# Kernel optimization log

Measured on AMD Instinct MI355X. Metric: run time of the kernel, lower is better.

Reference implementation:

```python
import jax, jax.numpy as jnp
import numpy as np

EPSILON = 1e-19
MASKING_RATIO = 0.75
N_BINS = 64
SIGMA = 0.01


def setup_inputs() -> dict:
    key = jax.random.key(0)
    k1, k2 = jax.random.split(key)
    N, L, D = 4, 512, 1024
    P = 768  # 16*16*3 pixels per patch
    x = jax.random.normal(k1, (N, L, D), dtype=jnp.float32)
    img_pat = jax.random.uniform(k2, (N, L, P), dtype=jnp.float32)
    return {"x": x, "img_pat": img_pat}


def _entropy_kde(values, n_bins=N_BINS, sigma=SIGMA):
    # values: [N, L, P]; global min/max normalization as in the torch code
    bins = jnp.linspace(0.0, 1.0, n_bins, dtype=values.dtype)  # [B]
    vmin = values.min()
    vmax = values.max()
    nv = (values - vmin) / (vmax - vmin)
    # residuals: [N, L, B, P]
    resid = nv[:, :, None, :] - bins[None, None, :, None]
    kern = jnp.exp(-0.5 * (resid / sigma) ** 2)
    pdf = kern.mean(axis=3)  # [N, L, B]
    pdf = pdf / (pdf.sum(axis=2, keepdims=True) + EPSILON) + EPSILON
    return -jnp.sum(pdf * jnp.log(pdf), axis=-1)  # [N, L]


def reference(x, img_pat):
    # entropy_kde_masking branch of MaskingModule.forward
    N, L, D = x.shape
    len_keep = int(L * (1.0 - MASKING_RATIO))
    entropies = _entropy_kde(img_pat)                 # [N, L]
    ids_shuffle = jnp.argsort(entropies, axis=1)      # ascending (descending=False)
    ids_restore = jnp.argsort(ids_shuffle, axis=1)    # [N, L]
    ids_keep = ids_shuffle[:, :len_keep]              # [N, len_keep]
    x_masked = jnp.take_along_axis(x, ids_keep[:, :, None], axis=1)  # [N, len_keep, D]
    mask = jnp.ones((N, L), dtype=x.dtype).at[:, :len_keep].set(0.0)
    mask = jnp.take_along_axis(mask, ids_restore, axis=1)
    return (x_masked, mask, ids_restore)
```

## Files before the change

### kernel.cpp

```cpp
#include <hip/hip_runtime.h>

#define NB 4
#define LB 512
#define DB 1024
#define PB 768
#define NBINS 64
#define LEN_KEEP 128
#define EPSL 1e-19f
#define WIN 3

#if defined(__has_builtin)
#if __has_builtin(__builtin_amdgcn_exp2f)
#define HAVE_EXP2 1
#endif
#endif

__device__ __forceinline__ float fast_exp2(float x) {
#ifdef HAVE_EXP2
    return __builtin_amdgcn_exp2f(x);
#else
    return __expf(x * 0.69314718055994530942f);
#endif
}

__global__ void minmax_partial(const float4* __restrict__ v,
                               float* __restrict__ bmin, float* __restrict__ bmax) {
    __shared__ float smin[256], smax[256];
    int tid = threadIdx.x;
    int base = blockIdx.x * 256 + tid;
    float mn = 1e30f, mx = -1e30f;
#pragma unroll
    for (int k = 0; k < 24; ++k) {
        float4 t4 = v[base + k * 16384];
        mn = fminf(mn, fminf(fminf(t4.x, t4.y), fminf(t4.z, t4.w)));
        mx = fmaxf(mx, fmaxf(fmaxf(t4.x, t4.y), fmaxf(t4.z, t4.w)));
    }
    smin[tid] = mn; smax[tid] = mx;
    __syncthreads();
    for (int s = 128; s > 0; s >>= 1) {
        if (tid < s) {
            smin[tid] = fminf(smin[tid], smin[tid + s]);
            smax[tid] = fmaxf(smax[tid], smax[tid + s]);
        }
        __syncthreads();
    }
    if (tid == 0) { bmin[blockIdx.x] = smin[0]; bmax[blockIdx.x] = smax[0]; }
}

__global__ void entropy_kernel(const float* __restrict__ img,
                               const float* __restrict__ bmin,
                               const float* __restrict__ bmax,
                               float* __restrict__ ent) {
    __shared__ float sh[256];
    __shared__ float snv[PB];
    __shared__ int   cnt[NBINS];
    __shared__ int   bs[NBINS + 1];
    __shared__ int   pos[NBINS];

    int t = blockIdx.x;
    int tid = threadIdx.x;
    int lane = tid & 63;
    int w = tid >> 6;

    if (tid < NBINS) cnt[tid] = 0;
    if (tid < 64) {
        float mn = bmin[tid], mx = bmax[tid];
        for (int m = 1; m < 64; m <<= 1) {
            mn = fminf(mn, __shfl_xor(mn, m, 64));
            mx = fmaxf(mx, __shfl_xor(mx, m, 64));
        }
        if (tid == 0) { sh[0] = mn; sh[1] = mx; }
    }
    __syncthreads();
    float vmin = sh[0], vmax = sh[1];
    float inv = 1.0f / (vmax - vmin);

    const float* row = img + (size_t)t * PB;
    float nv0 = (row[tid]       - vmin) * inv;
    float nv1 = (row[tid + 256] - vmin) * inv;
    float nv2 = (row[tid + 512] - vmin) * inv;
    int m0 = min(63, max(0, __float2int_rn(nv0 * 63.0f)));
    int m1 = min(63, max(0, __float2int_rn(nv1 * 63.0f)));
    int m2 = min(63, max(0, __float2int_rn(nv2 * 63.0f)));
    atomicAdd(&cnt[m0], 1);
    atomicAdd(&cnt[m1], 1);
    atomicAdd(&cnt[m2], 1);
    __syncthreads();

    if (tid < 64) {
        int c = cnt[tid];
        int incl = c;
        for (int off = 1; off < 64; off <<= 1) {
            int up = __shfl_up(incl, off, 64);
            if (tid >= off) incl += up;
        }
        bs[tid + 1] = incl;
        pos[tid] = incl - c;
        if (tid == 0) bs[0] = 0;
    }
    __syncthreads();

    snv[atomicAdd(&pos[m0], 1)] = nv0;
    snv[atomicAdd(&pos[m1], 1)] = nv1;
    snv[atomicAdd(&pos[m2], 1)] = nv2;
    __syncthreads();

    float bv = (float)lane * (1.0f / 63.0f);
    int lo = bs[max(0, lane - WIN)];
    int hi = bs[min(NBINS, lane + WIN + 1)];
    const float negC = -7213.4755859375f;
    float acc = 0.0f;
    for (int j = lo + w; j < hi; j += 4) {
        float d = snv[j] - bv;
        acc += fast_exp2(d * d * negC);
    }
    sh[w * NBINS + lane] = acc;
    __syncthreads();

    if (tid < 64) {
        float pdf = (sh[lane] + sh[64 + lane] + sh[128 + lane] + sh[192 + lane])
                    * (1.0f / (float)PB);
        float s = pdf;
        for (int m = 1; m < 64; m <<= 1) s += __shfl_xor(s, m, 64);
        float p = pdf / (s + EPSL) + EPSL;
        float term = p * __logf(p);
        for (int m = 1; m < 64; m <<= 1) term += __shfl_xor(term, m, 64);
        if (tid == 0) ent[t] = -term;
    }
}

__global__ void rank_gather_kernel(const float* __restrict__ x,
                                   const float* __restrict__ ent,
                                   float* __restrict__ out_x,
                                   float* __restrict__ out_mask,
                                   float* __restrict__ out_rest) {
    __shared__ float sh[LB];
    __shared__ int keep_list[16];
    __shared__ int nkeep;
    int b = blockIdx.x, tid = threadIdx.x;
    int n = b >> 5;
    int i = (b & 31) * 16 + (tid >> 4);
    int slice = tid & 15;

    if (tid == 0) nkeep = 0;
    sh[tid]       = ent[n * LB + tid];
    sh[256 + tid] = ent[n * LB + 256 + tid];
    __syncthreads();

    unsigned long long ci =
        ((unsigned long long)__float_as_uint(sh[i]) << 32) | (unsigned int)i;
    int r = 0;
    int j0 = slice * 32;
#pragma unroll 8
    for (int j = j0; j < j0 + 32; ++j) {
        unsigned long long cj =
            ((unsigned long long)__float_as_uint(sh[j]) << 32) | (unsigned int)j;
        r += (cj < ci) ? 1 : 0;
    }
    r += __shfl_xor(r, 1, 64);
    r += __shfl_xor(r, 2, 64);
    r += __shfl_xor(r, 4, 64);
    r += __shfl_xor(r, 8, 64);
    if (slice == 0) {
        out_rest[n * LB + i] = (float)r;
        out_mask[n * LB + i] = (r < LEN_KEEP) ? 0.0f : 1.0f;
        if (r < LEN_KEEP) {
            int e = atomicAdd(&nkeep, 1);
            keep_list[e] = (r << 16) | i;
        }
    }
    __syncthreads();

    int nk = nkeep;
    for (int e = 0; e < nk; ++e) {
        int ent_ri = keep_list[e];
        int slot = ent_ri >> 16;
        int rowi = ent_ri & 0xFFFF;
        const float4* src = (const float4*)(x + ((size_t)(n * LB + rowi)) * DB);
        float4* dst = (float4*)(out_x + ((size_t)(n * LEN_KEEP + slot)) * DB);
        dst[tid] = src[tid];
    }
}

extern "C" void kernel_launch(void* const* d_in, const int* in_sizes, int n_in,
                              void* d_out, int out_size, void* d_ws, size_t ws_size,
                              hipStream_t stream) {
    const float* x   = (const float*)d_in[0];
    const float* img = (const float*)d_in[1];

    float* out      = (float*)d_out;
    float* out_x    = out;
    float* out_mask = out + (size_t)NB * LEN_KEEP * DB;
    float* out_rest = out_mask + NB * LB;

    float* ws   = (float*)d_ws;
    float* bmin = ws;
    float* bmax = ws + 64;
    float* ent  = ws + 128;

    minmax_partial<<<64, 256, 0, stream>>>((const float4*)img, bmin, bmax);
    entropy_kernel<<<NB * LB, 256, 0, stream>>>(img, bmin, bmax, ent);
    rank_gather_kernel<<<128, 256, 0, stream>>>(x, ent, out_x, out_mask, out_rest);
}
```

Baseline: 75.83 us.

## Shrink entropy kernel to one wavefront per row

After: 80.72 us. +6.4%, slower.

```diff
diff --git a/kernel.cpp b/kernel.cpp
--- a/kernel.cpp
+++ b/kernel.cpp
@@ -47,62 +47,56 @@
     if (tid == 0) { bmin[blockIdx.x] = smin[0]; bmax[blockIdx.x] = smax[0]; }
 }
 
-__global__ void entropy_kernel(const float* __restrict__ img,
-                               const float* __restrict__ bmin,
-                               const float* __restrict__ bmax,
-                               float* __restrict__ ent) {
-    __shared__ float sh[256];
+__global__ __launch_bounds__(64) void entropy_kernel(
+    const float* __restrict__ img,
+    const float* __restrict__ bmin,
+    const float* __restrict__ bmax,
+    float* __restrict__ ent) {
     __shared__ float snv[PB];
     __shared__ int   cnt[NBINS];
     __shared__ int   bs[NBINS + 1];
     __shared__ int   pos[NBINS];
 
     int t = blockIdx.x;
-    int tid = threadIdx.x;
-    int lane = tid & 63;
-    int w = tid >> 6;
+    int lane = threadIdx.x;
 
-    if (tid < NBINS) cnt[tid] = 0;
-    if (tid < 64) {
-        float mn = bmin[tid], mx = bmax[tid];
-        for (int m = 1; m < 64; m <<= 1) {
-            mn = fminf(mn, __shfl_xor(mn, m, 64));
-            mx = fmaxf(mx, __shfl_xor(mx, m, 64));
-        }
-        if (tid == 0) { sh[0] = mn; sh[1] = mx; }
+    float vmin = bmin[lane], vmax = bmax[lane];
+    for (int m = 1; m < 64; m <<= 1) {
+        vmin = fminf(vmin, __shfl_xor(vmin, m, 64));
+        vmax = fmaxf(vmax, __shfl_xor(vmax, m, 64));
+    }
+    float inv = 1.0f / (vmax - vmin);
+
+    cnt[lane] = 0;
+    __syncthreads();
+
+    const float* row = img + (size_t)t * PB;
+    float nv[12];
+    int   mb[12];
+#pragma unroll
+    for (int k = 0; k < 12; ++k) {
+        nv[k] = (row[lane + 64 * k] - vmin) * inv;
+        mb[k] = min(63, max(0, __float2int_rn(nv[k] * 63.0f)));
+        atomicAdd(&cnt[mb[k]], 1);
     }
     __syncthreads();
-    float vmin = sh[0], vmax = sh[1];
-    float inv = 1.0f / (vmax - vmin);
 
-    const float* row = img + (size_t)t * PB;
-    float nv0 = (row[tid]       - vmin) * inv;
-    float nv1 = (row[tid + 256] - vmin) * inv;
-    float nv2 = (row[tid + 512] - vmin) * inv;
-    int m0 = min(63, max(0, __float2int_rn(nv0 * 63.0f)));
-    int m1 = min(63, max(0, __float2int_rn(nv1 * 63.0f)));
-    int m2 = min(63, max(0, __float2int_rn(nv2 * 63.0f)));
-    atomicAdd(&cnt[m0], 1);
-    atomicAdd(&cnt[m1], 1);
-    atomicAdd(&cnt[m2], 1);
-    __syncthreads();
-
-    if (tid < 64) {
-        int c = cnt[tid];
+    {
+        int c = cnt[lane];
         int incl = c;
         for (int off = 1; off < 64; off <<= 1) {
             int up = __shfl_up(incl, off, 64);
-            if (tid >= off) incl += up;
+            if (lane >= off) incl += up;
         }
-        bs[tid + 1] = incl;
-        pos[tid] = incl - c;
-        if (tid == 0) bs[0] = 0;
+        bs[lane + 1] = incl;
+        pos[lane] = incl - c;
+        if (lane == 0) bs[0] = 0;
     }
     __syncthreads();
 
-    snv[atomicAdd(&pos[m0], 1)] = nv0;
-    snv[atomicAdd(&pos[m1], 1)] = nv1;
-    snv[atomicAdd(&pos[m2], 1)] = nv2;
+#pragma unroll
+    for (int k = 0; k < 12; ++k)
+        snv[atomicAdd(&pos[mb[k]], 1)] = nv[k];
     __syncthreads();
 
     float bv = (float)lane * (1.0f / 63.0f);
@@ -110,23 +104,18 @@
     int hi = bs[min(NBINS, lane + WIN + 1)];
     const float negC = -7213.4755859375f;
     float acc = 0.0f;
-    for (int j = lo + w; j < hi; j += 4) {
+    for (int j = lo; j < hi; ++j) {
         float d = snv[j] - bv;
         acc += fast_exp2(d * d * negC);
     }
-    sh[w * NBINS + lane] = acc;
-    __syncthreads();
 
-    if (tid < 64) {
-        float pdf = (sh[lane] + sh[64 + lane] + sh[128 + lane] + sh[192 + lane])
-                    * (1.0f / (float)PB);
-        float s = pdf;
-        for (int m = 1; m < 64; m <<= 1) s += __shfl_xor(s, m, 64);
-        float p = pdf / (s + EPSL) + EPSL;
-        float term = p * __logf(p);
-        for (int m = 1; m < 64; m <<= 1) term += __shfl_xor(term, m, 64);
-        if (tid == 0) ent[t] = -term;
-    }
+    float pdf = acc * (1.0f / (float)PB);
+    float s = pdf;
+    for (int m = 1; m < 64; m <<= 1) s += __shfl_xor(s, m, 64);
+    float p = pdf / (s + EPSL) + EPSL;
+    float term = p * __logf(p);
+    for (int m = 1; m < 64; m <<= 1) term += __shfl_xor(term, m, 64);
+    if (lane == 0) ent[t] = -term;
 }
 
 __global__ void rank_gather_kernel(const float* __restrict__ x,
@@ -199,6 +188,6 @@
     float* ent  = ws + 128;
 
     minmax_partial<<<64, 256, 0, stream>>>((const float4*)img, bmin, bmax);
-    entropy_kernel<<<NB * LB, 256, 0, stream>>>(img, bmin, bmax, ent);
+    entropy_kernel<<<NB * LB, 64, 0, stream>>>(img, bmin, bmax, ent);
     rank_gather_kernel<<<128, 256, 0, stream>>>(x, ent, out_x, out_mask, out_rest);
 }
```
